# Performance work log

Hardware: AMD Instinct MI355X
Metric: run time of the kernel (lower is better)

## Reference

```python
import jax, jax.numpy as jnp
import numpy as np

NEG_INIT = -1.0e9


def setup_inputs() -> dict:
    key = jax.random.key(0)
    k1, k2, k3, k4, k5, k6, k7 = jax.random.split(key, 7)
    N, D, d_att, G = 262144, 512, 128, 512
    feats = jax.random.normal(k1, (N, D), dtype=jnp.float32)
    index = jnp.sort(jax.random.randint(k2, (N,), 0, G, dtype=jnp.int64))
    # torch Linear params: weight (out,in), bias (out,)
    Vw = jax.random.normal(k3, (d_att, D), dtype=jnp.float32) / np.sqrt(D)
    Vb = jax.random.normal(k4, (d_att,), dtype=jnp.float32) * 0.01
    Uw = jax.random.normal(k5, (d_att, D), dtype=jnp.float32) / np.sqrt(D)
    Ub = jax.random.normal(k6, (d_att,), dtype=jnp.float32) * 0.01
    ww = jax.random.normal(k7, (1, d_att), dtype=jnp.float32) / np.sqrt(d_att)
    return {"feats": feats, "index": index, "num_groups": G,
            "Vw": Vw, "Vb": Vb, "Uw": Uw, "Ub": Ub, "ww": ww}


def reference(feats, index, num_groups, Vw, Vb, Uw, Ub, ww):
    # gated attention MLP: A = tanh(V x) * sigmoid(U x); scores = w A
    A = jnp.tanh(feats @ Vw.T + Vb) * jax.nn.sigmoid(feats @ Uw.T + Ub)  # (N, d_att)
    scores = (A @ ww.T)[:, 0]  # (N,)
    # segment max with -1e9 init (matches scatter_reduce amax include_self)
    max_per_group = jax.ops.segment_max(scores, index, num_segments=num_groups)
    max_per_group = jnp.maximum(max_per_group, NEG_INIT)  # empty segments -> -1e9
    exp_scores = jnp.exp(scores - max_per_group[index])
    denom = jax.ops.segment_sum(exp_scores, index, num_segments=num_groups)
    weights = exp_scores / (denom[index] + 1e-8)
    # weighted scatter-sum pooling: (num_groups, D)
    out = jax.ops.segment_sum(feats * weights[:, None], index, num_segments=num_groups)
    return out
```

## Files before the change

kernel.cpp:

```cpp
#include <hip/hip_runtime.h>
#include <hip/hip_fp8.h>
#include <cstddef>

#define NEG_INIT -1.0e9f

typedef _Float16 f16x8 __attribute__((ext_vector_type(8)));
typedef _Float16 f16x4 __attribute__((ext_vector_type(4)));
typedef float f32x4 __attribute__((ext_vector_type(4)));

constexpr int D   = 512;
constexpr int BM  = 32;
constexpr int BK  = 32;
constexpr int NKS = D / BK;
constexpr int SSK = 4;
constexpr int NSS = NKS / SSK;
constexpr int LDH  = 520;
constexpr int LDRB = 520;
constexpr int PS  = 516;
constexpr float RSC  = 2048.f;
constexpr float RISC = 1.f / 2048.f;

#define BAR_LGKM()                                            \
    do {                                                      \
        asm volatile("s_waitcnt lgkmcnt(0)" ::: "memory");    \
        __builtin_amdgcn_s_barrier();                         \
        asm volatile("" ::: "memory");                        \
    } while (0)

#if __has_builtin(__builtin_amdgcn_cvt_pk_fp8_f32) && __has_builtin(__builtin_amdgcn_cvt_f32_fp8)
#define HW_FP8 1
#else
#define HW_FP8 0
#endif

__device__ __forceinline__ unsigned int pack_fp8x4(float r0, float r1,
                                                   float r2, float r3) {
#if HW_FP8
    int p = __builtin_amdgcn_cvt_pk_fp8_f32(r0, r1, 0, false);
    p     = __builtin_amdgcn_cvt_pk_fp8_f32(r2, r3, p, true);
    return (unsigned int)p;
#else
    __hip_fp8_e4m3 q0(r0), q1(r1), q2(r2), q3(r3);
    return (unsigned int)q0.__x | ((unsigned int)q1.__x << 8) |
           ((unsigned int)q2.__x << 16) | ((unsigned int)q3.__x << 24);
#endif
}

template <int SEL>
__device__ __forceinline__ float unpack_fp8(unsigned int word) {
#if HW_FP8
    return __builtin_amdgcn_cvt_f32_fp8((int)word, SEL);
#else
    __hip_fp8_e4m3 q;
    q.__x = (unsigned char)(word >> (8 * SEL));
    return (float)q;
#endif
}

__device__ __forceinline__ float fast_tanh(float v) {
    float e2 = __expf(2.f * v);
    return 1.f - 2.f * __builtin_amdgcn_rcpf(e2 + 1.f);
}
__device__ __forceinline__ float fast_sigmoid(float u) {
    return __builtin_amdgcn_rcpf(1.f + __expf(-u));
}

__global__ __launch_bounds__(64) void k_wprep(const float* __restrict__ Vw,
                                              const float* __restrict__ Uw,
                                              _Float16* __restrict__ Wfrag) {
    const int bid  = blockIdx.x;
    const int lane = threadIdx.x;
    const int j    = bid & 3;
    const int ks   = (bid >> 2) & 15;
    const int wc   = bid >> 6;
    const int l15  = lane & 15;
    const int kgrp = lane >> 4;
    const float* src = (j < 2 ? Vw + (size_t)(wc * 32 + j * 16 + l15) * D
                              : Uw + (size_t)(wc * 32 + (j - 2) * 16 + l15) * D)
                       + ks * BK + kgrp * 8;
    f16x8 h;
    #pragma unroll
    for (int e = 0; e < 8; ++e) h[e] = (_Float16)src[e];
    *(f16x8*)(Wfrag + ((size_t)bid * 64 + lane) * 8) = h;
}

__global__ __launch_bounds__(256) void k_bounds(const int* __restrict__ index,
                                                int N, int G,
                                                int* __restrict__ start) {
    int g = blockIdx.x * blockDim.x + threadIdx.x;
    if (g > G) return;
    int lo = 0, hi = N;
    while (lo < hi) {
        int mid = (lo + hi) >> 1;
        if (index[mid] < g) lo = mid + 1; else hi = mid;
    }
    start[g] = lo;
}

__global__ __launch_bounds__(512, 6) void k_fused(
    const float* __restrict__ feats, const _Float16* __restrict__ Wfrag,
    const float* __restrict__ Vb, const float* __restrict__ Ub,
    const float* __restrict__ ww, const int* __restrict__ index,
    const int* __restrict__ start, float* __restrict__ P, int N)
{
    __shared__ __align__(16) _Float16 Xh[BM][LDH];
    __shared__ __align__(8)  unsigned char Xr8[BM * LDRB];
    __shared__ float sred[8][BM];
    __shared__ float srow[BM];
    __shared__ float evals[BM];

    const int t    = threadIdx.x;
    const int lane = t & 63;
    const int wc   = t >> 6;
    const int l15  = lane & 15;
    const int kgrp = lane >> 4;
    const int blk  = blockIdx.x;
    const int rb   = blk * BM;

    const int srw  = t >> 4;
    const int scol = (t & 15) * 8;
    const float* xg = feats + (size_t)(rb + srw) * D + scol;

    float4 xa[3][2];
    auto issueX = [&](int ss) {
        const float* p = xg + ss * 128;
        const int sl = ss % 3;
        xa[sl][0] = *(const float4*)p;
        xa[sl][1] = *(const float4*)(p + 4);
    };
    auto commitX = [&](int ss) {
        const int c0 = ss * 128 + scol;
        const int sl = ss % 3;
        float v[8];
        v[0] = xa[sl][0].x; v[1] = xa[sl][0].y;
        v[2] = xa[sl][0].z; v[3] = xa[sl][0].w;
        v[4] = xa[sl][1].x; v[5] = xa[sl][1].y;
        v[6] = xa[sl][1].z; v[7] = xa[sl][1].w;
        f16x8 h;
        float res[8];
        #pragma unroll
        for (int e = 0; e < 8; ++e) {
            h[e] = (_Float16)v[e];
            res[e] = (v[e] - (float)h[e]) * RSC;
        }
        unsigned int rp0 = pack_fp8x4(res[0], res[1], res[2], res[3]);
        unsigned int rp1 = pack_fp8x4(res[4], res[5], res[6], res[7]);
        *(f16x8*)&Xh[srw][c0] = h;
        uint2 rw = {rp0, rp1};
        *(uint2*)&Xr8[srw * LDRB + c0] = rw;
    };

    const _Float16* wbV = Wfrag + (size_t)(wc >> 1) * 32768
                                + (size_t)(wc & 1) * 512 + (size_t)lane * 8;
    const _Float16* wbU = wbV + 1024;

    f32x4 accV[2], accU[2];
    #pragma unroll
    for (int i = 0; i < 2; ++i) {
        accV[i] = (f32x4){0.f, 0.f, 0.f, 0.f};
        accU[i] = (f32x4){0.f, 0.f, 0.f, 0.f};
    }

    issueX(0); issueX(1); issueX(2);
    commitX(0);
    BAR_LGKM();

    #pragma unroll
    for (int ss = 0; ss < NSS; ++ss) {
        if (ss + 3 < NSS) issueX(ss + 3);
        #pragma unroll
        for (int k2 = 0; k2 < SSK; ++k2) {
            const int ks = ss * SSK + k2;
            f16x8 bv = *(const f16x8*)(wbV + (size_t)ks * 2048);
            f16x8 bu = *(const f16x8*)(wbU + (size_t)ks * 2048);
            f16x8 ha[2];
            #pragma unroll
            for (int i = 0; i < 2; ++i)
                ha[i] = *(const f16x8*)&Xh[i * 16 + l15][ks * BK + kgrp * 8];
            #pragma unroll
            for (int i = 0; i < 2; ++i) {
                accV[i] = __builtin_amdgcn_mfma_f32_16x16x32_f16(ha[i], bv, accV[i], 0, 0, 0);
                accU[i] = __builtin_amdgcn_mfma_f32_16x16x32_f16(ha[i], bu, accU[i], 0, 0, 0);
            }
        }
        if (ss + 1 < NSS) {
            commitX(ss + 1);
            BAR_LGKM();
        }
    }

    {
        const int c = wc * 16 + l15;
        const float vb = Vb[c], ub = Ub[c], w = ww[c];
        float part[2][4];
        #pragma unroll
        for (int i = 0; i < 2; ++i)
            #pragma unroll
            for (int r = 0; r < 4; ++r) {
                float v = accV[i][r] + vb;
                float u = accU[i][r] + ub;
                part[i][r] = w * fast_tanh(v) * fast_sigmoid(u);
            }
        #pragma unroll
        for (int off = 1; off < 16; off <<= 1)
            #pragma unroll
            for (int i = 0; i < 2; ++i)
                #pragma unroll
                for (int r = 0; r < 4; ++r)
                    part[i][r] += __shfl_xor(part[i][r], off);
        if (l15 == 0) {
            #pragma unroll
            for (int i = 0; i < 2; ++i)
                #pragma unroll
                for (int r = 0; r < 4; ++r)
                    sred[wc][i * 16 + kgrp * 4 + r] = part[i][r];
        }
    }
    __syncthreads();
    if (t < BM) {
        float s = sred[0][t];
        #pragma unroll
        for (int w8 = 1; w8 < 8; ++w8) s += sred[w8][t];
        srow[t] = s;
    }
    __syncthreads();

    const int gl = index[rb];
    const int gh = index[rb + BM - 1];
    for (int g = gl + wc; g <= gh; g += 8) {
        const int r0 = max(start[g], rb), r1 = min(start[g + 1], rb + BM);
        if (r1 <= r0) continue;
        const bool in = (lane >= r0 - rb) && (lane < r1 - rb);
        float m = in ? srow[lane] : NEG_INIT;
        #pragma unroll
        for (int off = 32; off; off >>= 1) m = fmaxf(m, __shfl_xor(m, off));
        float e = in ? __expf(srow[lane] - m) : 0.f;
        if (in) evals[lane] = e;
        float s = e;
        #pragma unroll
        for (int off = 32; off; off >>= 1) s += __shfl_xor(s, off);
        if (lane == 0) {
            float* slot = P + (size_t)(blk + g) * PS;
            slot[0] = m; slot[1] = s;
        }
    }
    __syncthreads();

    {
        for (int g = gl; g <= gh; ++g) {
            const int r0 = max(start[g], rb), r1 = min(start[g + 1], rb + BM);
            if (r1 <= r0) continue;
            float a = 0.f;
            for (int r = r0; r < r1; ++r) {
                const int rr = r - rb;
                float h = (float)Xh[rr][t];
                unsigned int rv = Xr8[rr * LDRB + t];
                float x = fmaf(unpack_fp8<0>(rv), RISC, h);
                a = fmaf(evals[rr], x, a);
            }
            P[(size_t)(blk + g) * PS + 4 + t] = a;
        }
    }
}

__global__ __launch_bounds__(512) void k_merge(const float* __restrict__ P,
                                               const int* __restrict__ start,
                                               float* __restrict__ out)
{
    const int g = blockIdx.x, t = threadIdx.x;
    const int s0 = start[g], s1 = start[g + 1];
    if (s0 >= s1) { out[(size_t)g * D + t] = 0.f; return; }
    const int b0 = s0 >> 5, b1 = (s1 - 1) >> 5;
    float M = NEG_INIT;
    for (int b = b0; b <= b1; ++b)
        M = fmaxf(M, P[(size_t)(b + g) * PS]);
    float den = 0.f, acc = 0.f;
    for (int b = b0; b <= b1; ++b) {
        const float* slot = P + (size_t)(b + g) * PS;
        float w = __expf(slot[0] - M);
        den += w * slot[1];
        acc += w * slot[4 + t];
    }
    out[(size_t)g * D + t] = acc / (den + 1e-8f);
}

extern "C" void kernel_launch(void* const* d_in, const int* in_sizes, int n_in,
                              void* d_out, int out_size, void* d_ws, size_t ws_size,
                              hipStream_t stream) {
    const float* feats = (const float*)d_in[0];
    const int*   index = (const int*)d_in[1];
    const float* Vw = (const float*)d_in[3];
    const float* Vb = (const float*)d_in[4];
    const float* Uw = (const float*)d_in[5];
    const float* Ub = (const float*)d_in[6];
    const float* ww = (const float*)d_in[7];
    float* out = (float*)d_out;

    const int N = in_sizes[1];
    const int G = out_size / D;
    const int nblk = (N + BM - 1) / BM;

    _Float16* Wfrag = (_Float16*)d_ws;
    int* start      = (int*)(Wfrag + (size_t)256 * 512);
    size_t off      = (size_t)256 * 512 * 2 + (G + 1) * 4;
    off             = (off + 15) & ~(size_t)15;
    float* P        = (float*)((char*)d_ws + off);

    hipLaunchKernelGGL(k_wprep, dim3(256), dim3(64), 0, stream, Vw, Uw, Wfrag);
    hipLaunchKernelGGL(k_bounds, dim3((G + 1 + 255) / 256), dim3(256), 0, stream,
                       index, N, G, start);
    hipLaunchKernelGGL(k_fused, dim3(nblk), dim3(512), 0, stream,
                       feats, Wfrag, Vb, Ub, ww, index, start, P, N);
    hipLaunchKernelGGL(k_merge, dim3(G), dim3(512), 0, stream, P, start, out);
}
```

Baseline: 209.8 us.

## Batch weight loads per stage and shrink X prefetch to one stage ahead

Drops the three-deep register ring for feature prefetch and keeps only one stage in flight. All four k-step weight fragments for a stage are now loaded up front, fenced with sched_barrier so the weight loads are issued ahead of the next X prefetch. This cuts register pressure and groups the weight loads, but leaves less lookahead to hide global feature-load latency.

```diff
diff --git a/kernel.cpp b/kernel.cpp
--- a/kernel.cpp
+++ b/kernel.cpp
@@ -5,7 +5,6 @@
 #define NEG_INIT -1.0e9f
 
 typedef _Float16 f16x8 __attribute__((ext_vector_type(8)));
-typedef _Float16 f16x4 __attribute__((ext_vector_type(4)));
 typedef float f32x4 __attribute__((ext_vector_type(4)));
 
 constexpr int D   = 512;
@@ -121,21 +120,17 @@
     const int scol = (t & 15) * 8;
     const float* xg = feats + (size_t)(rb + srw) * D + scol;
 
-    float4 xa[3][2];
+    float4 xa0, xa1;
     auto issueX = [&](int ss) {
         const float* p = xg + ss * 128;
-        const int sl = ss % 3;
-        xa[sl][0] = *(const float4*)p;
-        xa[sl][1] = *(const float4*)(p + 4);
+        xa0 = *(const float4*)p;
+        xa1 = *(const float4*)(p + 4);
     };
     auto commitX = [&](int ss) {
         const int c0 = ss * 128 + scol;
-        const int sl = ss % 3;
         float v[8];
-        v[0] = xa[sl][0].x; v[1] = xa[sl][0].y;
-        v[2] = xa[sl][0].z; v[3] = xa[sl][0].w;
-        v[4] = xa[sl][1].x; v[5] = xa[sl][1].y;
-        v[6] = xa[sl][1].z; v[7] = xa[sl][1].w;
+        v[0] = xa0.x; v[1] = xa0.y; v[2] = xa0.z; v[3] = xa0.w;
+        v[4] = xa1.x; v[5] = xa1.y; v[6] = xa1.z; v[7] = xa1.w;
         f16x8 h;
         float res[8];
         #pragma unroll
@@ -161,26 +156,33 @@
         accU[i] = (f32x4){0.f, 0.f, 0.f, 0.f};
     }
 
-    issueX(0); issueX(1); issueX(2);
+    issueX(0);
     commitX(0);
     BAR_LGKM();
 
     #pragma unroll
     for (int ss = 0; ss < NSS; ++ss) {
-        if (ss + 3 < NSS) issueX(ss + 3);
+        f16x8 bv[SSK], bu[SSK];
         #pragma unroll
         for (int k2 = 0; k2 < SSK; ++k2) {
             const int ks = ss * SSK + k2;
-            f16x8 bv = *(const f16x8*)(wbV + (size_t)ks * 2048);
-            f16x8 bu = *(const f16x8*)(wbU + (size_t)ks * 2048);
+            bv[k2] = *(const f16x8*)(wbV + (size_t)ks * 2048);
+            bu[k2] = *(const f16x8*)(wbU + (size_t)ks * 2048);
+        }
+        __builtin_amdgcn_sched_barrier(0);
+        if (ss + 1 < NSS) issueX(ss + 1);
+        __builtin_amdgcn_sched_barrier(0);
+        #pragma unroll
+        for (int k2 = 0; k2 < SSK; ++k2) {
+            const int ks = ss * SSK + k2;
             f16x8 ha[2];
             #pragma unroll
             for (int i = 0; i < 2; ++i)
                 ha[i] = *(const f16x8*)&Xh[i * 16 + l15][ks * BK + kgrp * 8];
             #pragma unroll
             for (int i = 0; i < 2; ++i) {
-                accV[i] = __builtin_amdgcn_mfma_f32_16x16x32_f16(ha[i], bv, accV[i], 0, 0, 0);
-                accU[i] = __builtin_amdgcn_mfma_f32_16x16x32_f16(ha[i], bu, accU[i], 0, 0, 0);
+                accV[i] = __builtin_amdgcn_mfma_f32_16x16x32_f16(ha[i], bv[k2], accV[i], 0, 0, 0);
+                accU[i] = __builtin_amdgcn_mfma_f32_16x16x32_f16(ha[i], bu[k2], accU[i], 0, 0, 0);
             }
         }
         if (ss + 1 < NSS) {
```

Result: no change. 213.6 us (+1.8%).
